# Optimization experiments

Hardware: AMD Instinct MI355X
Metric: run time of the kernel (lower is better)

Reference implementation:

```python
import jax, jax.numpy as jnp
import numpy as np

B, T, C = 1, 4096, 1024
H = 16
D = C // H  # head_dim = 64


def setup_inputs() -> dict:
    key = jax.random.key(0)
    ks = jax.random.split(key, 9)
    s = 1.0 / np.sqrt(C)
    return {
        "x": jax.random.normal(ks[0], (B, T, C), dtype=jnp.float32),
        "Wq": jax.random.normal(ks[1], (C, C), dtype=jnp.float32) * s,
        "bq": jnp.zeros((C,), dtype=jnp.float32),
        "Wk": jax.random.normal(ks[2], (C, C), dtype=jnp.float32) * s,
        "bk": jnp.zeros((C,), dtype=jnp.float32),
        "Wv": jax.random.normal(ks[3], (C, C), dtype=jnp.float32) * s,
        "bv": jnp.zeros((C,), dtype=jnp.float32),
        "Wo": jax.random.normal(ks[4], (C, C), dtype=jnp.float32) * s,
        "bo": jnp.zeros((C,), dtype=jnp.float32),
    }


def reference(x, Wq, bq, Wk, bk, Wv, bv, Wo, bo):
    # QKV projections (torch Linear: y = x @ W.T + b)
    q = x @ Wq.T + bq
    k = x @ Wk.T + bk
    v = x @ Wv.T + bv
    # [B,T,C] -> [B,H,T,D]
    q = q.reshape(B, T, H, D).transpose(0, 2, 1, 3)
    k = k.reshape(B, T, H, D).transpose(0, 2, 1, 3)
    v = v.reshape(B, T, H, D).transpose(0, 2, 1, 3)
    scale = 1.0 / jnp.sqrt(jnp.asarray(D, dtype=q.dtype))
    scores = jnp.einsum("bhqd,bhkd->bhqk", q, k) * scale  # [B,H,T,T]
    attn = jax.nn.softmax(scores, axis=-1)
    out = jnp.einsum("bhqk,bhkd->bhqd", attn, v)  # [B,H,T,D]
    out = out.transpose(0, 2, 1, 3).reshape(B, T, C)
    return out @ Wo.T + bo
```

## Files before the change

### kernel.cpp

```cpp
#include <hip/hip_runtime.h>
#include <stdint.h>

#define T_SEQ 4096
#define CDIM  1024
#define NH    16
#define DH    64

typedef _Float16 half8 __attribute__((ext_vector_type(8)));
typedef _Float16 half4 __attribute__((ext_vector_type(4)));
typedef float    f32x4 __attribute__((ext_vector_type(4)));

#if __has_builtin(__builtin_amdgcn_exp2f)
#define EXP2F(x) __builtin_amdgcn_exp2f(x)
#else
#define EXP2F(x) exp2f(x)
#endif

#define MFMA_K32(a, b, c) __builtin_amdgcn_mfma_f32_16x16x32_f16(a, b, c, 0, 0, 0)

__device__ __forceinline__ uint32_t pk2(float a, float b) {
  auto h = __builtin_amdgcn_cvt_pkrtz(a, b);
  return __builtin_bit_cast(uint32_t, h);
}

__device__ __forceinline__ void gl_lds16(const void* g, void* l) {
  __builtin_amdgcn_global_load_lds(
      (const __attribute__((address_space(1))) uint32_t*)g,
      (__attribute__((address_space(3))) uint32_t*)l, 16, 0, 0);
}

__global__ void cvt_all_kernel(const float* __restrict__ w0, const float* __restrict__ w1,
                               const float* __restrict__ w2, const float* __restrict__ w3,
                               const float* __restrict__ x,
                               _Float16* __restrict__ o0, _Float16* __restrict__ o1,
                               _Float16* __restrict__ o2, _Float16* __restrict__ o3,
                               _Float16* __restrict__ xo) {
  int y = blockIdx.y;
  const float* src;
  _Float16* dst;
  if (y < 4) {
    src = (y == 0) ? w0 : (y == 1) ? w1 : (y == 2) ? w2 : w3;
    dst = (y == 0) ? o0 : (y == 1) ? o1 : (y == 2) ? o2 : o3;
  } else {
    src = x  + (size_t)(y - 4) * (CDIM * CDIM);
    dst = xo + (size_t)(y - 4) * (CDIM * CDIM);
  }
  int i = (blockIdx.x * blockDim.x + threadIdx.x) * 8;
  float4 f0 = *(const float4*)(src + i);
  float4 f1 = *(const float4*)(src + i + 4);
  half8 h = { (_Float16)f0.x, (_Float16)f0.y, (_Float16)f0.z, (_Float16)f0.w,
              (_Float16)f1.x, (_Float16)f1.y, (_Float16)f1.z, (_Float16)f1.w };
  *(half8*)(dst + i) = h;
}

__device__ __forceinline__ void gemm_core(const _Float16* __restrict__ A,
                                          const _Float16* __restrict__ Bm,
                                          _Float16* As, _Float16* Bs,
                                          int bm, int bn,
                                          f32x4 (&acc)[4][4]) {
  const int tid  = threadIdx.x;
  const int lane = tid & 63;
  const int wave = tid >> 6;
  const int waveM = wave >> 1, waveN = wave & 1;
  const int quad = lane >> 4, c16 = lane & 15;

  const int rs0 = wave * 32 + (lane >> 2);
  const int rs1 = rs0 + 16;
  const int dm0 = ((lane & 3) ^ ((rs0 >> 1) & 3)) * 8;
  const int dm1 = ((lane & 3) ^ ((rs1 >> 1) & 3)) * 8;

  const _Float16* gA0 = A  + (size_t)(bm * 128 + rs0) * CDIM + dm0;
  const _Float16* gA1 = A  + (size_t)(bm * 128 + rs1) * CDIM + dm1;
  const _Float16* gB0 = Bm + (size_t)(bn * 128 + rs0) * CDIM + dm0;
  const _Float16* gB1 = Bm + (size_t)(bn * 128 + rs1) * CDIM + dm1;
  _Float16* lA0 = As + wave * 1024;
  _Float16* lA1 = lA0 + 512;
  _Float16* lB0 = Bs + wave * 1024;
  _Float16* lB1 = lB0 + 512;

  const int xsw  = (c16 >> 1) & 3;
  const int offA = (waveM * 64 + c16) * 32 + ((quad ^ xsw) * 8);
  const int offB = (waveN * 64 + c16) * 32 + ((quad ^ xsw) * 8);

  for (int kk = 0; kk < 32; ++kk) {
    gl_lds16(gA0, lA0);
    gl_lds16(gA1, lA1);
    gl_lds16(gB0, lB0);
    gl_lds16(gB1, lB1);
    __syncthreads();
    half8 a[4], b[4];
#pragma unroll
    for (int i = 0; i < 4; ++i) a[i] = *(const half8*)(As + offA + i * 512);
#pragma unroll
    for (int i = 0; i < 4; ++i) b[i] = *(const half8*)(Bs + offB + i * 512);
#pragma unroll
    for (int mi = 0; mi < 4; ++mi)
#pragma unroll
      for (int ni = 0; ni < 4; ++ni)
        acc[mi][ni] = MFMA_K32(a[mi], b[ni], acc[mi][ni]);
    gA0 += 32; gA1 += 32; gB0 += 32; gB1 += 32;
    __syncthreads();
  }
}

__device__ __forceinline__ void gemm_core64(const _Float16* __restrict__ A,
                                            const _Float16* __restrict__ Bm,
                                            _Float16* As, _Float16* Bs,
                                            int bm, int bn,
                                            f32x4 (&acc)[2][4]) {
  const int tid  = threadIdx.x;
  const int lane = tid & 63;
  const int wave = tid >> 6;
  const int waveM = wave >> 1, waveN = wave & 1;
  const int quad = lane >> 4, c16 = lane & 15;

  const int rsA = wave * 16 + (lane >> 2);
  const int dmA = ((lane & 3) ^ ((rsA >> 1) & 3)) * 8;
  const int rs0 = wave * 32 + (lane >> 2);
  const int rs1 = rs0 + 16;
  const int dm0 = ((lane & 3) ^ ((rs0 >> 1) & 3)) * 8;
  const int dm1 = ((lane & 3) ^ ((rs1 >> 1) & 3)) * 8;

  const _Float16* gA0 = A  + (size_t)(bm * 64  + rsA) * CDIM + dmA;
  const _Float16* gB0 = Bm + (size_t)(bn * 128 + rs0) * CDIM + dm0;
  const _Float16* gB1 = Bm + (size_t)(bn * 128 + rs1) * CDIM + dm1;
  _Float16* lA0 = As + wave * 512;
  _Float16* lB0 = Bs + wave * 1024;
  _Float16* lB1 = lB0 + 512;

  const int xsw  = (c16 >> 1) & 3;
  const int offA = (waveM * 32 + c16) * 32 + ((quad ^ xsw) * 8);
  const int offB = (waveN * 64 + c16) * 32 + ((quad ^ xsw) * 8);

  for (int kk = 0; kk < 32; ++kk) {
    gl_lds16(gA0, lA0);
    gl_lds16(gB0, lB0);
    gl_lds16(gB1, lB1);
    __syncthreads();
    half8 a[2], b[4];
#pragma unroll
    for (int i = 0; i < 2; ++i) a[i] = *(const half8*)(As + offA + i * 512);
#pragma unroll
    for (int i = 0; i < 4; ++i) b[i] = *(const half8*)(Bs + offB + i * 512);
#pragma unroll
    for (int mi = 0; mi < 2; ++mi)
#pragma unroll
      for (int ni = 0; ni < 4; ++ni)
        acc[mi][ni] = MFMA_K32(a[mi], b[ni], acc[mi][ni]);
    gA0 += 32; gB0 += 32; gB1 += 32;
    __syncthreads();
  }
}

__global__ __launch_bounds__(256) void qkv_gemm(
    const _Float16* __restrict__ xh,
    const _Float16* __restrict__ wqh, const _Float16* __restrict__ wkh, const _Float16* __restrict__ wvh,
    const float* __restrict__ bq, const float* __restrict__ bk, const float* __restrict__ bv,
    _Float16* __restrict__ qh, _Float16* __restrict__ kh, _Float16* __restrict__ vth) {
  __shared__ __align__(16) _Float16 As[128 * 32];
  __shared__ __align__(16) _Float16 Bs[128 * 32];
  const int z = blockIdx.z;
  const _Float16* W   = (z == 0) ? wqh : ((z == 1) ? wkh : wvh);
  const float*    bias = (z == 0) ? bq  : ((z == 1) ? bk  : bv);

  f32x4 acc[4][4];
  const f32x4 zf = {0.f, 0.f, 0.f, 0.f};
#pragma unroll
  for (int i = 0; i < 4; ++i)
#pragma unroll
    for (int j = 0; j < 4; ++j) acc[i][j] = zf;

  gemm_core(xh, W, As, Bs, blockIdx.x, blockIdx.y, acc);

  const int lane = threadIdx.x & 63, wave = threadIdx.x >> 6;
  const int waveM = wave >> 1, waveN = wave & 1;
  const int quad = lane >> 4, c16 = lane & 15;
  const int rowb = blockIdx.x * 128 + waveM * 64;
  const int colb = blockIdx.y * 128 + waveN * 64;

  float bsv[4];
#pragma unroll
  for (int ni = 0; ni < 4; ++ni) bsv[ni] = bias[colb + ni * 16 + c16];

  if (z < 2) {
    _Float16* outp = (z == 0) ? qh : kh;
    const float scl = (z == 0) ? 0.18033688011112042f : 1.0f;
#pragma unroll
    for (int mi = 0; mi < 4; ++mi)
#pragma unroll
      for (int ni = 0; ni < 4; ++ni) {
        int col = colb + ni * 16 + c16;
        int hh = col >> 6, dd = col & 63;
#pragma unroll
        for (int r = 0; r < 4; ++r) {
          int row = rowb + mi * 16 + quad * 4 + r;
          outp[(size_t)(hh * T_SEQ + row) * DH + dd] = (_Float16)((acc[mi][ni][r] + bsv[ni]) * scl);
        }
      }
  } else {
#pragma unroll
    for (int mi = 0; mi < 4; ++mi)
#pragma unroll
      for (int ni = 0; ni < 4; ++ni) {
        int col  = colb + ni * 16 + c16;
        int row0 = rowb + mi * 16 + quad * 4;
        half4 h4;
#pragma unroll
        for (int r = 0; r < 4; ++r) h4[r] = (_Float16)(acc[mi][ni][r] + bsv[ni]);
        *(half4*)(vth + (size_t)col * T_SEQ + row0) = h4;
      }
  }
}

__global__ __launch_bounds__(256) void out_gemm(
    const _Float16* __restrict__ ctx, const _Float16* __restrict__ woh,
    const float* __restrict__ bo, float* __restrict__ out) {
  __shared__ __align__(16) _Float16 As[64 * 32];
  __shared__ __align__(16) _Float16 Bs[128 * 32];
  f32x4 acc[2][4];
  const f32x4 zf = {0.f, 0.f, 0.f, 0.f};
#pragma unroll
  for (int i = 0; i < 2; ++i)
#pragma unroll
    for (int j = 0; j < 4; ++j) acc[i][j] = zf;

  gemm_core64(ctx, woh, As, Bs, blockIdx.x, blockIdx.y, acc);

  const int lane = threadIdx.x & 63, wave = threadIdx.x >> 6;
  const int waveM = wave >> 1, waveN = wave & 1;
  const int quad = lane >> 4, c16 = lane & 15;
  const int rowb = blockIdx.x * 64 + waveM * 32;
  const int colb = blockIdx.y * 128 + waveN * 64;

  float bsv[4];
#pragma unroll
  for (int ni = 0; ni < 4; ++ni) bsv[ni] = bo[colb + ni * 16 + c16];

#pragma unroll
  for (int mi = 0; mi < 2; ++mi)
#pragma unroll
    for (int ni = 0; ni < 4; ++ni) {
      int col = colb + ni * 16 + c16;
#pragma unroll
      for (int r = 0; r < 4; ++r) {
        int row = rowb + mi * 16 + quad * 4 + r;
        out[(size_t)row * CDIM + col] = acc[mi][ni][r] + bsv[ni];
      }
    }
}

__global__ __launch_bounds__(256, 2) void attn_kernel(
    const _Float16* __restrict__ qh, const _Float16* __restrict__ kh,
    const _Float16* __restrict__ vth, _Float16* __restrict__ ctx) {
  __shared__ __align__(16) _Float16 Ks[4][64 * 64];
  __shared__ __align__(16) _Float16 Vs[4][64 * 64];

  const int tid = threadIdx.x, lane = tid & 63, wave = tid >> 6;
  const int quad = lane >> 4, c16 = lane & 15;
  const int l  = blockIdx.y * 32 + blockIdx.x;
  const int w  = (l & 7) * 64 + (l >> 3);
  const int h  = w >> 5;
  const int qw = (w & 31) * 128 + wave * 32;

  half8 qf[2][2];
#pragma unroll
  for (int qg = 0; qg < 2; ++qg)
#pragma unroll
    for (int c = 0; c < 2; ++c)
      qf[qg][c] = *(const half8*)(qh + (size_t)(h * T_SEQ + qw + qg * 16 + c16) * DH + c * 32 + quad * 8);

  const int rs0 = wave * 16 + (lane >> 3);
  const int rs1 = rs0 + 8;
  const int dm0 = ((lane & 7) ^ (rs0 & 7)) * 8;
  const int dm1 = ((lane & 7) ^ (rs1 & 7)) * 8;
  const _Float16* gK0 = kh  + (size_t)(h * T_SEQ + rs0) * DH + dm0;
  const _Float16* gK1 = kh  + (size_t)(h * T_SEQ + rs1) * DH + dm1;
  const _Float16* gV0 = vth + (size_t)(h * DH + rs0) * T_SEQ + dm0;
  const _Float16* gV1 = vth + (size_t)(h * DH + rs1) * T_SEQ + dm1;
  const int lo0 = wave * 1024, lo1 = wave * 1024 + 512;

  f32x4 o[2][4];
  f32x4 lacc[2];
  const f32x4 zf = {0.f, 0.f, 0.f, 0.f};
#pragma unroll
  for (int qg = 0; qg < 2; ++qg) {
#pragma unroll
    for (int db = 0; db < 4; ++db) o[qg][db] = zf;
    lacc[qg] = zf;
  }
  const half8 ones8 = { (_Float16)1, (_Float16)1, (_Float16)1, (_Float16)1,
                        (_Float16)1, (_Float16)1, (_Float16)1, (_Float16)1 };

  auto stage = [&](int b) {
    gl_lds16(gK0, &Ks[b][lo0]);
    gl_lds16(gK1, &Ks[b][lo1]);
    gl_lds16(gV0, &Vs[b][lo0]);
    gl_lds16(gV1, &Vs[b][lo1]);
    gK0 += 64 * DH; gK1 += 64 * DH; gV0 += 64; gV1 += 64;
  };

  union U8 { uint32_t u[4]; half8 h; };

  auto compute = [&](int bc) {
    const _Float16* Kb = &Ks[bc][0];
    const _Float16* Vb = &Vs[bc][0];

    const f32x4 minit = {-16.f, -16.f, -16.f, -16.f};
    f32x4 s[2][4];
#pragma unroll
    for (int qg = 0; qg < 2; ++qg)
#pragma unroll
      for (int kb = 0; kb < 4; ++kb) s[qg][kb] = minit;
    __builtin_amdgcn_s_setprio(1);
#pragma unroll
    for (int c = 0; c < 2; ++c) {
#pragma unroll
      for (int kb = 0; kb < 4; ++kb) {
        int key = kb * 16 + c16;
        half8 ak = *(const half8*)(Kb + key * 64 + (((c * 4 + quad) ^ (key & 7)) * 8));
        s[0][kb] = MFMA_K32(ak, qf[0][c], s[0][kb]);
        s[1][kb] = MFMA_K32(ak, qf[1][c], s[1][kb]);
      }
    }
    __builtin_amdgcn_s_setprio(0);

    half8 bp[2][2];
#pragma unroll
    for (int qg = 0; qg < 2; ++qg) {
      float p[4][4];
#pragma unroll
      for (int kb = 0; kb < 4; ++kb)
#pragma unroll
        for (int r = 0; r < 4; ++r) p[kb][r] = EXP2F(s[qg][kb][r]);
#pragma unroll
      for (int kb32 = 0; kb32 < 2; ++kb32) {
        uint32_t a0 = pk2(p[2 * kb32][0],     p[2 * kb32][1]);
        uint32_t a1 = pk2(p[2 * kb32][2],     p[2 * kb32][3]);
        uint32_t b0 = pk2(p[2 * kb32 + 1][0], p[2 * kb32 + 1][1]);
        uint32_t b1 = pk2(p[2 * kb32 + 1][2], p[2 * kb32 + 1][3]);
        asm("v_permlane32_swap_b32 %0, %1" : "+v"(a0), "+v"(b0));
        asm("v_permlane16_swap_b32 %0, %1" : "+v"(a0), "+v"(b0));
        asm("v_permlane32_swap_b32 %0, %1" : "+v"(a1), "+v"(b1));
        asm("v_permlane16_swap_b32 %0, %1" : "+v"(a1), "+v"(b1));
        U8 u;
        u.u[0] = a0; u.u[1] = a1; u.u[2] = b0; u.u[3] = b1;
        bp[qg][kb32] = u.h;
      }
    }

    __builtin_amdgcn_s_setprio(1);
#pragma unroll
    for (int kb32 = 0; kb32 < 2; ++kb32) {
      half8 av[4];
#pragma unroll
      for (int db = 0; db < 4; ++db) {
        int d = db * 16 + c16;
        av[db] = *(const half8*)(Vb + d * 64 + (((kb32 * 4 + quad) ^ (d & 7)) * 8));
      }
#pragma unroll
      for (int qg = 0; qg < 2; ++qg) {
        lacc[qg] = MFMA_K32(ones8, bp[qg][kb32], lacc[qg]);
#pragma unroll
        for (int db = 0; db < 4; ++db)
          o[qg][db] = MFMA_K32(av[db], bp[qg][kb32], o[qg][db]);
      }
    }
    __builtin_amdgcn_s_setprio(0);
  };

  stage(0);
  stage(1);
  __syncthreads();

  for (int jj = 0; jj < 16; ++jj) {
    stage(2); stage(3);
    compute(0); compute(1);
    __syncthreads();
    if (jj < 15) { stage(0); stage(1); }
    compute(2); compute(3);
    __syncthreads();
  }

  _Float16* Pw = &Ks[0][0] + wave * 2048;
#pragma unroll
  for (int qg = 0; qg < 2; ++qg) {
    float inv = 1.f / lacc[qg][0];
#pragma unroll
    for (int db = 0; db < 4; ++db) {
      half4 h4;
#pragma unroll
      for (int r = 0; r < 4; ++r) h4[r] = (_Float16)(o[qg][db][r] * inv);
      int row = qg * 16 + c16;
      int g   = db * 2 + (quad >> 1);
      *(half4*)(Pw + row * 64 + ((g ^ (row & 7)) * 8) + (quad & 1) * 4) = h4;
    }
  }
  const int q = lane >> 1, hv = lane & 1;
#pragma unroll
  for (int i = 0; i < 4; ++i) {
    int g = hv * 4 + i;
    half8 vv = *(const half8*)(Pw + q * 64 + ((g ^ (q & 7)) * 8));
    *(half8*)(ctx + (size_t)(qw + q) * CDIM + h * DH + g * 8) = vv;
  }
}

extern "C" void kernel_launch(void* const* d_in, const int* in_sizes, int n_in,
                              void* d_out, int out_size, void* d_ws, size_t ws_size,
                              hipStream_t stream) {
  const float* x  = (const float*)d_in[0];
  const float* Wq = (const float*)d_in[1];
  const float* bq = (const float*)d_in[2];
  const float* Wk = (const float*)d_in[3];
  const float* bk = (const float*)d_in[4];
  const float* Wv = (const float*)d_in[5];
  const float* bv = (const float*)d_in[6];
  const float* Wo = (const float*)d_in[7];
  const float* bo = (const float*)d_in[8];
  float* out = (float*)d_out;

  char* ws = (char*)d_ws;
  _Float16* xh  = (_Float16*)(ws);
  _Float16* qh  = (_Float16*)(ws + ((size_t)8  << 20));
  _Float16* kh  = (_Float16*)(ws + ((size_t)16 << 20));
  _Float16* vth = (_Float16*)(ws + ((size_t)24 << 20));
  _Float16* wqh = (_Float16*)(ws + ((size_t)32 << 20));
  _Float16* wkh = (_Float16*)(ws + ((size_t)34 << 20));
  _Float16* wvh = (_Float16*)(ws + ((size_t)36 << 20));
  _Float16* woh = (_Float16*)(ws + ((size_t)38 << 20));
  _Float16* ctx = xh;

  cvt_all_kernel<<<dim3(512, 8), 256, 0, stream>>>(Wq, Wk, Wv, Wo, x,
                                                   wqh, wkh, wvh, woh, xh);
  qkv_gemm<<<dim3(32, 8, 3), 256, 0, stream>>>(xh, wqh, wkh, wvh, bq, bk, bv, qh, kh, vth);
  attn_kernel<<<dim3(32, 16), 256, 0, stream>>>(qh, kh, vth, ctx);
  out_gemm<<<dim3(64, 8), 256, 0, stream>>>(ctx, woh, bo, out);
}
```

Baseline: 213.4 us.

## Double-buffer LDS tiles in QKV and output projection GEMMs

Both GEMM cores now use two LDS buffers. The next k-slice's global-to-LDS load is issued before the MFMAs on the current slice, and one barrier is dropped per iteration. This is meant to hide global load latency behind compute in the projection GEMMs. LDS use per block doubles, which may reduce occupancy. The attention kernel, likely the dominant cost, is unchanged.

```diff
diff --git a/kernel.cpp b/kernel.cpp
--- a/kernel.cpp
+++ b/kernel.cpp
@@ -73,32 +73,38 @@
   const _Float16* gA1 = A  + (size_t)(bm * 128 + rs1) * CDIM + dm1;
   const _Float16* gB0 = Bm + (size_t)(bn * 128 + rs0) * CDIM + dm0;
   const _Float16* gB1 = Bm + (size_t)(bn * 128 + rs1) * CDIM + dm1;
-  _Float16* lA0 = As + wave * 1024;
-  _Float16* lA1 = lA0 + 512;
-  _Float16* lB0 = Bs + wave * 1024;
-  _Float16* lB1 = lB0 + 512;
+  const int lw = wave * 1024;
 
   const int xsw  = (c16 >> 1) & 3;
   const int offA = (waveM * 64 + c16) * 32 + ((quad ^ xsw) * 8);
   const int offB = (waveN * 64 + c16) * 32 + ((quad ^ xsw) * 8);
 
+  auto stageT = [&](int b) {
+    _Float16* bA = As + b * 4096;
+    _Float16* bB = Bs + b * 4096;
+    gl_lds16(gA0, bA + lw);
+    gl_lds16(gA1, bA + lw + 512);
+    gl_lds16(gB0, bB + lw);
+    gl_lds16(gB1, bB + lw + 512);
+    gA0 += 32; gA1 += 32; gB0 += 32; gB1 += 32;
+  };
+
+  stageT(0);
+  __syncthreads();
   for (int kk = 0; kk < 32; ++kk) {
-    gl_lds16(gA0, lA0);
-    gl_lds16(gA1, lA1);
-    gl_lds16(gB0, lB0);
-    gl_lds16(gB1, lB1);
-    __syncthreads();
+    if (kk < 31) stageT((kk + 1) & 1);
+    const _Float16* cA = As + (kk & 1) * 4096;
+    const _Float16* cB = Bs + (kk & 1) * 4096;
     half8 a[4], b[4];
 #pragma unroll
-    for (int i = 0; i < 4; ++i) a[i] = *(const half8*)(As + offA + i * 512);
-#pragma unroll
-    for (int i = 0; i < 4; ++i) b[i] = *(const half8*)(Bs + offB + i * 512);
+    for (int i = 0; i < 4; ++i) a[i] = *(const half8*)(cA + offA + i * 512);
+#pragma unroll
+    for (int i = 0; i < 4; ++i) b[i] = *(const half8*)(cB + offB + i * 512);
 #pragma unroll
     for (int mi = 0; mi < 4; ++mi)
 #pragma unroll
       for (int ni = 0; ni < 4; ++ni)
         acc[mi][ni] = MFMA_K32(a[mi], b[ni], acc[mi][ni]);
-    gA0 += 32; gA1 += 32; gB0 += 32; gB1 += 32;
     __syncthreads();
   }
 }
@@ -124,30 +130,36 @@
   const _Float16* gA0 = A  + (size_t)(bm * 64  + rsA) * CDIM + dmA;
   const _Float16* gB0 = Bm + (size_t)(bn * 128 + rs0) * CDIM + dm0;
   const _Float16* gB1 = Bm + (size_t)(bn * 128 + rs1) * CDIM + dm1;
-  _Float16* lA0 = As + wave * 512;
-  _Float16* lB0 = Bs + wave * 1024;
-  _Float16* lB1 = lB0 + 512;
 
   const int xsw  = (c16 >> 1) & 3;
   const int offA = (waveM * 32 + c16) * 32 + ((quad ^ xsw) * 8);
   const int offB = (waveN * 64 + c16) * 32 + ((quad ^ xsw) * 8);
 
+  auto stageT = [&](int b) {
+    _Float16* bA = As + b * 2048;
+    _Float16* bB = Bs + b * 4096;
+    gl_lds16(gA0, bA + wave * 512);
+    gl_lds16(gB0, bB + wave * 1024);
+    gl_lds16(gB1, bB + wave * 1024 + 512);
+    gA0 += 32; gB0 += 32; gB1 += 32;
+  };
+
+  stageT(0);
+  __syncthreads();
   for (int kk = 0; kk < 32; ++kk) {
-    gl_lds16(gA0, lA0);
-    gl_lds16(gB0, lB0);
-    gl_lds16(gB1, lB1);
-    __syncthreads();
+    if (kk < 31) stageT((kk + 1) & 1);
+    const _Float16* cA = As + (kk & 1) * 2048;
+    const _Float16* cB = Bs + (kk & 1) * 4096;
     half8 a[2], b[4];
 #pragma unroll
-    for (int i = 0; i < 2; ++i) a[i] = *(const half8*)(As + offA + i * 512);
-#pragma unroll
-    for (int i = 0; i < 4; ++i) b[i] = *(const half8*)(Bs + offB + i * 512);
+    for (int i = 0; i < 2; ++i) a[i] = *(const half8*)(cA + offA + i * 512);
+#pragma unroll
+    for (int i = 0; i < 4; ++i) b[i] = *(const half8*)(cB + offB + i * 512);
 #pragma unroll
     for (int mi = 0; mi < 2; ++mi)
 #pragma unroll
       for (int ni = 0; ni < 4; ++ni)
         acc[mi][ni] = MFMA_K32(a[mi], b[ni], acc[mi][ni]);
-    gA0 += 32; gB0 += 32; gB1 += 32;
     __syncthreads();
   }
 }
@@ -157,8 +169,8 @@
     const _Float16* __restrict__ wqh, const _Float16* __restrict__ wkh, const _Float16* __restrict__ wvh,
     const float* __restrict__ bq, const float* __restrict__ bk, const float* __restrict__ bv,
     _Float16* __restrict__ qh, _Float16* __restrict__ kh, _Float16* __restrict__ vth) {
-  __shared__ __align__(16) _Float16 As[128 * 32];
-  __shared__ __align__(16) _Float16 Bs[128 * 32];
+  __shared__ __align__(16) _Float16 As[2 * 128 * 32];
+  __shared__ __align__(16) _Float16 Bs[2 * 128 * 32];
   const int z = blockIdx.z;
   const _Float16* W   = (z == 0) ? wqh : ((z == 1) ? wkh : wvh);
   const float*    bias = (z == 0) ? bq  : ((z == 1) ? bk  : bv);
@@ -215,8 +227,8 @@
 __global__ __launch_bounds__(256) void out_gemm(
     const _Float16* __restrict__ ctx, const _Float16* __restrict__ woh,
     const float* __restrict__ bo, float* __restrict__ out) {
-  __shared__ __align__(16) _Float16 As[64 * 32];
-  __shared__ __align__(16) _Float16 Bs[128 * 32];
+  __shared__ __align__(16) _Float16 As[2 * 64 * 32];
+  __shared__ __align__(16) _Float16 Bs[2 * 128 * 32];
   f32x4 acc[2][4];
   const f32x4 zf = {0.f, 0.f, 0.f, 0.f};
 #pragma unroll
```

Measured after the change: 220.3 us. 3.3% more time.
